# Kernel tuning notes

Hardware: AMD Instinct MI355X
Metric: run time of the kernel (lower is better)

The kernel has to match this reference:

```python
import jax, jax.numpy as jnp
import numpy as np
from jax import lax

jax.config.update("jax_enable_x64", True)

# physical constants / module hyperparameters (match Photodetector defaults)
Q = 1.602176563e-19          # electron charge
KB = 1.3806488e-23           # Boltzmann constant
T_KELVIN = 300.0
BITRATE = 5.0e10
DARK_CURRENT = 1e-10
LOAD_R = 1.0e6
RESPONSIVITY = 1.0
ORDER = 4
WN = 25.0e9 / (0.5 / 1e-12)  # bandwidth / nyquist = 0.05


def _butter_lowpass(order, wn):
    """Digital Butterworth lowpass (b, a), identical algorithm to scipy.signal.butter."""
    warped = 4.0 * np.tan(np.pi * wn / 2.0)          # pre-warped analog cutoff (fs=2)
    kk = np.arange(1, order + 1)
    p = warped * np.exp(1j * np.pi * (2 * kk + order - 1) / (2.0 * order))  # analog poles
    gain = warped ** order
    fs2 = 4.0                                        # 2*fs with fs=2 (bilinear)
    pz = (fs2 + p) / (fs2 - p)                       # digital poles
    gz = gain * np.real(1.0 / np.prod(fs2 - p))      # digital gain (no analog zeros)
    b = np.real(gz * np.poly(-np.ones(order)))       # zeros at z=-1
    a = np.real(np.poly(pz))
    return b, a


def setup_inputs() -> dict:
    key = jax.random.key(0)
    k1, k2 = jax.random.split(key)
    T_steps, B = 16384, 512
    Kf = ORDER + 1
    signal = jax.random.uniform(k1, (T_steps, B), dtype=jnp.float32)  # optical power >= 0
    noise = jax.random.normal(k2, (B, 1, T_steps + Kf - 1), dtype=jnp.float32)
    b, a = _butter_lowpass(ORDER, WN)
    return {
        "signal": signal,
        "noise": noise,
        "b": jnp.asarray(b, jnp.float64),
        "a_rev": jnp.asarray(a[::-1].copy(), jnp.float64),  # module stores a reversed
    }


def reference(signal, noise, b, a_rev):
    sig = signal.astype(jnp.float64)            # (T, B)
    K = b.shape[0]
    x = sig.T                                   # (B, T)
    xp = jnp.pad(x, ((0, 0), (K - 1, 0)))       # left-pad K-1 zeros -> (B, Tp)
    # shot + thermal noise std, batch-mean of signal per timestep
    mean_sig = jnp.mean(RESPONSIVITY * xp, axis=0)  # (Tp,)
    noise_sd = jnp.sqrt(2.0 * Q * BITRATE * (mean_sig + DARK_CURRENT)
                        + 4.0 * KB * T_KELVIN * BITRATE / LOAD_R)
    xn = noise_sd * noise[:, 0, :].astype(jnp.float64) + RESPONSIVITY * xp  # (B, Tp)
    # FIR (torch Conv1d = cross-correlation, matched by lax conv)
    y = lax.conv_general_dilated(xn[:, None, :], b[None, None, :],
                                 window_strides=(1,), padding="VALID")  # (B,1,T)
    s = y[:, 0, :].T                             # (T, B)
    # IIR recurrence: first N samples pass through, then y[n] = s[n] - sum a_rev[:-1]*y[n-N+1:n]
    N = a_rev.shape[0]
    coefs = a_rev[:-1]                           # (N-1,), a_rev[-1] == a[0] == 1

    def step(carry, sn):                         # carry: (N-1, B) = y[n-N+1 .. n-1]
        yn = sn - jnp.sum(coefs[:, None] * carry, axis=0)
        return jnp.concatenate([carry[1:], yn[None]], axis=0), yn

    _, ys = lax.scan(step, s[1:N], s[N:])
    out = jnp.concatenate([s[:N], ys], axis=0)   # (T, B)
    return out.astype(jnp.float32)
```

## Files before the change

kernel.cpp:

```cpp
#include <hip/hip_runtime.h>
#include <math.h>
#include <complex>

#define T_STEPS 16384
#define BATCH   512
#define KF      5
#define TAU     (T_STEPS + KF - 1)
#define NCHUNK  512
#define CHLEN   (T_STEPS / NCHUNK)
#define NTAU    (CHLEN + KF - 1)
#define NSER    12

struct Coefs {
    double b0, b1, b2, b3, b4;
    double c0, c1, c2, c3;
};
struct Mat { double m[16]; };

__device__ __forceinline__ int swz_chunk(int w) { return (w & 7) * (NCHUNK / 8) + (w >> 3); }

__global__ __launch_bounds__(512, 4) void k_stage(const float* __restrict__ signal,
                                                  const float* __restrict__ noise,
                                                  const Coefs k,
                                                  float* __restrict__ sbuf,
                                                  double* __restrict__ pend) {
    __shared__ float  part[NTAU * 8];
    __shared__ double sdsh[NTAU];

    const int tid = threadIdx.x;
    const int b   = tid;
    const int w   = tid >> 6;
    const int l   = tid & 63;
    const int c   = swz_chunk(blockIdx.x);
    const int t0  = c * CHLEN;

    const float4* nb = (const float4*)(noise + (size_t)b * TAU + t0);
    float4 nr[9];
    #pragma unroll
    for (int q = 0; q < 9; ++q) nr[q] = nb[q];
    float nv[NTAU];
    #pragma unroll
    for (int q = 0; q < 9; ++q) {
        nv[4 * q + 0] = nr[q].x; nv[4 * q + 1] = nr[q].y;
        nv[4 * q + 2] = nr[q].z; nv[4 * q + 3] = nr[q].w;
    }

    float sval[NTAU];
    #pragma unroll
    for (int j = 0; j < NTAU; ++j) {
        const int tau = t0 + j;
        sval[j] = (c == 0 && tau < 4) ? 0.0f : signal[(size_t)(tau - 4) * BATCH + b];
    }

    #pragma unroll
    for (int j = 0; j < NTAU; ++j) {
        float v = sval[j];
        for (int off = 32; off > 0; off >>= 1) v += __shfl_down(v, off, 64);
        if (l == 0) part[j * 8 + w] = v;
    }
    __syncthreads();
    if (tid < NTAU) {
        const double c1 = 2.0 * 1.602176563e-19 * 50000000000.0;
        const double c2 = 4.0 * 1.3806488e-23 * 300.0 * 50000000000.0 / 1000000.0;
        double ssum = 0.0;
        #pragma unroll
        for (int i = 0; i < 8; ++i) ssum += (double)part[tid * 8 + i];
        sdsh[tid] = sqrt(c1 * (ssum / 512.0 + 1e-10) + c2);
    }
    __syncthreads();

    auto XN = [&](int j) -> double {
        return sdsh[j] * (double)nv[j] + (double)sval[j];
    };
    double w0 = XN(0), w1 = XN(1), w2 = XN(2), w3 = XN(3), w4;
    double z0 = 0.0, z1 = 0.0, z2 = 0.0, z3 = 0.0;
    #pragma unroll
    for (int i = 0; i < CHLEN; ++i) {
        w4 = XN(i + 4);
        const double s = k.b0 * w0 + k.b1 * w1 + k.b2 * w2 + k.b3 * w3 + k.b4 * w4;
        sbuf[(size_t)(t0 + i) * BATCH + b] = (float)s;
        const double y = (c == 0 && i < 5) ? s
                       : s - (k.c0 * z0 + k.c1 * z1 + k.c2 * z2 + k.c3 * z3);
        z0 = z1; z1 = z2; z2 = z3; z3 = y;
        w0 = w1; w1 = w2; w2 = w3; w3 = w4;
    }
    pend[(size_t)(c * 4 + 0) * BATCH + b] = z0;
    pend[(size_t)(c * 4 + 1) * BATCH + b] = z1;
    pend[(size_t)(c * 4 + 2) * BATCH + b] = z2;
    pend[(size_t)(c * 4 + 3) * BATCH + b] = z3;
}

__global__ __launch_bounds__(256) void k_apply(const float* __restrict__ sbuf,
                                               const Coefs k,
                                               const Mat M,
                                               const double* __restrict__ pend,
                                               float* __restrict__ out) {
    const int b  = (int)blockIdx.y * 256 + threadIdx.x;
    const int c  = swz_chunk(blockIdx.x);
    const int t0 = c * CHLEN;

    double z0 = 0.0, z1 = 0.0, z2 = 0.0, z3 = 0.0;
    #pragma unroll
    for (int d = NSER; d >= 1; --d) {
        if (d <= c) {
            const int j = c - d;
            const double p0 = pend[(size_t)(j * 4 + 0) * BATCH + b];
            const double p1 = pend[(size_t)(j * 4 + 1) * BATCH + b];
            const double p2 = pend[(size_t)(j * 4 + 2) * BATCH + b];
            const double p3 = pend[(size_t)(j * 4 + 3) * BATCH + b];
            const double n0 = p0 + M.m[0] * z0 + M.m[4] * z1 + M.m[8]  * z2 + M.m[12] * z3;
            const double n1 = p1 + M.m[1] * z0 + M.m[5] * z1 + M.m[9]  * z2 + M.m[13] * z3;
            const double n2 = p2 + M.m[2] * z0 + M.m[6] * z1 + M.m[10] * z2 + M.m[14] * z3;
            const double n3 = p3 + M.m[3] * z0 + M.m[7] * z1 + M.m[11] * z2 + M.m[15] * z3;
            z0 = n0; z1 = n1; z2 = n2; z3 = n3;
        }
    }

    #pragma unroll
    for (int i = 0; i < CHLEN; ++i) {
        const double s = (double)sbuf[(size_t)(t0 + i) * BATCH + b];
        const double y = (c == 0 && i < 5) ? s
                       : s - (k.c0 * z0 + k.c1 * z1 + k.c2 * z2 + k.c3 * z3);
        z0 = z1; z1 = z2; z2 = z3; z3 = y;
        out[(size_t)(t0 + i) * BATCH + b] = (float)y;
    }
}

static Coefs make_coefs() {
    const int order = 4;
    const double wn = 25000000000.0 / (0.5 / 1e-12);
    const double warped = 4.0 * tan(M_PI * wn / 2.0);
    std::complex<double> p[4];
    for (int kk = 1; kk <= order; ++kk)
        p[kk - 1] = warped * std::exp(std::complex<double>(0.0,
                        M_PI * (2 * kk + order - 1) / (2.0 * order)));
    const double gain = warped * warped * warped * warped;
    const double fs2 = 4.0;
    std::complex<double> pz[4], prod(1.0, 0.0);
    for (int i = 0; i < 4; ++i) {
        pz[i] = (fs2 + p[i]) / (fs2 - p[i]);
        prod *= (fs2 - p[i]);
    }
    const double gz = gain * std::real(std::complex<double>(1.0, 0.0) / prod);
    std::complex<double> ac[5] = { {1,0}, {0,0}, {0,0}, {0,0}, {0,0} };
    for (int i = 0; i < 4; ++i)
        for (int j = i + 1; j >= 1; --j)
            ac[j] = ac[j] - pz[i] * ac[j - 1];
    Coefs k;
    k.b0 = gz * 1.0; k.b1 = gz * 4.0; k.b2 = gz * 6.0; k.b3 = gz * 4.0; k.b4 = gz * 1.0;
    k.c0 = std::real(ac[4]);
    k.c1 = std::real(ac[3]);
    k.c2 = std::real(ac[2]);
    k.c3 = std::real(ac[1]);
    return k;
}

static void mat_compose(const double* P, const double* Q, double* R) {
    double t[16];
    for (int j = 0; j < 4; ++j)
        for (int i = 0; i < 4; ++i) {
            double s = 0.0;
            for (int kk = 0; kk < 4; ++kk) s += P[j * 4 + kk] * Q[kk * 4 + i];
            t[j * 4 + i] = s;
        }
    for (int i = 0; i < 16; ++i) R[i] = t[i];
}

static Mat make_M(const Coefs& k) {
    double S[16] = {0};
    S[1 * 4 + 0] = 1.0;
    S[2 * 4 + 1] = 1.0;
    S[3 * 4 + 2] = 1.0;
    S[0 * 4 + 3] = -k.c0;
    S[1 * 4 + 3] = -k.c1;
    S[2 * 4 + 3] = -k.c2;
    S[3 * 4 + 3] = -k.c3;
    Mat M;
    double I[16] = {1,0,0,0, 0,1,0,0, 0,0,1,0, 0,0,0,1};
    for (int i = 0; i < 16; ++i) M.m[i] = I[i];
    for (int i = 0; i < CHLEN; ++i) mat_compose(M.m, S, M.m);
    return M;
}

extern "C" void kernel_launch(void* const* d_in, const int* in_sizes, int n_in,
                              void* d_out, int out_size, void* d_ws, size_t ws_size,
                              hipStream_t stream) {
    const float* signal = (const float*)d_in[0];
    const float* noise  = (const float*)d_in[1];
    float* out = (float*)d_out;

    const Coefs k = make_coefs();
    const Mat   M = make_M(k);

    char* ws = (char*)d_ws;
    float*  sbuf = (float*)ws;
    double* pend = (double*)(ws + 33554432);

    hipLaunchKernelGGL(k_stage, dim3(NCHUNK), dim3(512), 0, stream,
                       signal, noise, k, sbuf, pend);
    hipLaunchKernelGGL(k_apply, dim3(NCHUNK, 2), dim3(256), 0, stream,
                       sbuf, k, M, pend, out);
}
```

Measured before the change: 46.62 us.

## Fuse stage and apply kernels with cooperative grid sync and LDS-resident FIR output

Merges the two-kernel chunked IIR scan into one cooperative kernel. The FIR output stays in LDS (64 KB per block) across a grid-wide sync instead of round-tripping through a global scratch buffer, and the per-chunk carry states are stored as float4 instead of four doubles. This removes the second launch and the global write and re-read of the intermediate signal. In exchange it depends on all 512 blocks being co-resident (at least 2 per CU, checked at runtime with a two-kernel fallback), pays for a grid barrier, and rounds the carry states to float precision.

```diff
diff --git a/kernel.cpp b/kernel.cpp
--- a/kernel.cpp
+++ b/kernel.cpp
@@ -1,4 +1,5 @@
 #include <hip/hip_runtime.h>
+#include <hip/hip_cooperative_groups.h>
 #include <math.h>
 #include <complex>
 
@@ -17,7 +18,103 @@
 };
 struct Mat { double m[16]; };
 
+namespace cg = cooperative_groups;
+
 __device__ __forceinline__ int swz_chunk(int w) { return (w & 7) * (NCHUNK / 8) + (w >> 3); }
+
+__global__ __launch_bounds__(512, 4) void k_fused(const float* __restrict__ signal,
+                                                  const float* __restrict__ noise,
+                                                  const Coefs k,
+                                                  const Mat M,
+                                                  float4* __restrict__ pend4,
+                                                  float* __restrict__ out) {
+    __shared__ float  slds[BATCH * CHLEN];
+    __shared__ float  part[NTAU * 8];
+    __shared__ double sdsh[NTAU];
+
+    const int tid = threadIdx.x;
+    const int b   = tid;
+    const int w   = tid >> 6;
+    const int l   = tid & 63;
+    const int c   = swz_chunk(blockIdx.x);
+    const int t0  = c * CHLEN;
+
+    float sval[NTAU];
+    #pragma unroll
+    for (int j = 0; j < NTAU; ++j) {
+        const int tau = t0 + j;
+        sval[j] = (c == 0 && tau < 4) ? 0.0f : signal[(size_t)(tau - 4) * BATCH + b];
+    }
+
+    #pragma unroll
+    for (int j = 0; j < NTAU; ++j) {
+        float v = sval[j];
+        for (int off = 32; off > 0; off >>= 1) v += __shfl_down(v, off, 64);
+        if (l == 0) part[j * 8 + w] = v;
+    }
+    __syncthreads();
+    if (tid < NTAU) {
+        const double c1 = 2.0 * 1.602176563e-19 * 50000000000.0;
+        const double c2 = 4.0 * 1.3806488e-23 * 300.0 * 50000000000.0 / 1000000.0;
+        double ssum = 0.0;
+        #pragma unroll
+        for (int i = 0; i < 8; ++i) ssum += (double)part[tid * 8 + i];
+        sdsh[tid] = sqrt(c1 * (ssum / 512.0 + 1e-10) + c2);
+    }
+    __syncthreads();
+
+    const float4* nb = (const float4*)(noise + (size_t)b * TAU + t0);
+    double z0 = 0.0, z1 = 0.0, z2 = 0.0, z3 = 0.0;
+    {
+        float4 f = nb[0];
+        double w0 = sdsh[0] * (double)f.x + (double)sval[0];
+        double w1 = sdsh[1] * (double)f.y + (double)sval[1];
+        double w2 = sdsh[2] * (double)f.z + (double)sval[2];
+        double w3 = sdsh[3] * (double)f.w + (double)sval[3];
+        #pragma unroll
+        for (int q = 1; q < 9; ++q) {
+            f = nb[q];
+            const float nf[4] = { f.x, f.y, f.z, f.w };
+            #pragma unroll
+            for (int u = 0; u < 4; ++u) {
+                const int i = 4 * (q - 1) + u;
+                const int j = 4 * q + u;
+                const double w4 = sdsh[j] * (double)nf[u] + (double)sval[j];
+                const double s = k.b0 * w0 + k.b1 * w1 + k.b2 * w2 + k.b3 * w3 + k.b4 * w4;
+                slds[i * BATCH + b] = (float)s;
+                const double y = (c == 0 && i < 5) ? s
+                               : s - (k.c0 * z0 + k.c1 * z1 + k.c2 * z2 + k.c3 * z3);
+                z0 = z1; z1 = z2; z2 = z3; z3 = y;
+                w0 = w1; w1 = w2; w2 = w3; w3 = w4;
+            }
+        }
+    }
+    pend4[(size_t)c * BATCH + b] = make_float4((float)z0, (float)z1, (float)z2, (float)z3);
+
+    cg::this_grid().sync();
+
+    z0 = 0.0; z1 = 0.0; z2 = 0.0; z3 = 0.0;
+    #pragma unroll
+    for (int d = NSER; d >= 1; --d) {
+        if (d <= c) {
+            const float4 p = pend4[(size_t)(c - d) * BATCH + b];
+            const double n0 = (double)p.x + M.m[0] * z0 + M.m[4] * z1 + M.m[8]  * z2 + M.m[12] * z3;
+            const double n1 = (double)p.y + M.m[1] * z0 + M.m[5] * z1 + M.m[9]  * z2 + M.m[13] * z3;
+            const double n2 = (double)p.z + M.m[2] * z0 + M.m[6] * z1 + M.m[10] * z2 + M.m[14] * z3;
+            const double n3 = (double)p.w + M.m[3] * z0 + M.m[7] * z1 + M.m[11] * z2 + M.m[15] * z3;
+            z0 = n0; z1 = n1; z2 = n2; z3 = n3;
+        }
+    }
+
+    #pragma unroll
+    for (int i = 0; i < CHLEN; ++i) {
+        const double s = (double)slds[i * BATCH + b];
+        const double y = (c == 0 && i < 5) ? s
+                       : s - (k.c0 * z0 + k.c1 * z1 + k.c2 * z2 + k.c3 * z3);
+        z0 = z1; z1 = z2; z2 = z3; z3 = y;
+        out[(size_t)(t0 + i) * BATCH + b] = (float)y;
+    }
+}
 
 __global__ __launch_bounds__(512, 4) void k_stage(const float* __restrict__ signal,
                                                   const float* __restrict__ noise,
@@ -26,13 +123,10 @@
                                                   double* __restrict__ pend) {
     __shared__ float  part[NTAU * 8];
     __shared__ double sdsh[NTAU];
-
     const int tid = threadIdx.x;
-    const int b   = tid;
-    const int w   = tid >> 6;
-    const int l   = tid & 63;
-    const int c   = swz_chunk(blockIdx.x);
-    const int t0  = c * CHLEN;
+    const int b = tid, w = tid >> 6, l = tid & 63;
+    const int c = swz_chunk(blockIdx.x);
+    const int t0 = c * CHLEN;
 
     const float4* nb = (const float4*)(noise + (size_t)b * TAU + t0);
     float4 nr[9];
@@ -41,17 +135,14 @@
     float nv[NTAU];
     #pragma unroll
     for (int q = 0; q < 9; ++q) {
-        nv[4 * q + 0] = nr[q].x; nv[4 * q + 1] = nr[q].y;
-        nv[4 * q + 2] = nr[q].z; nv[4 * q + 3] = nr[q].w;
-    }
-
+        nv[4*q+0] = nr[q].x; nv[4*q+1] = nr[q].y; nv[4*q+2] = nr[q].z; nv[4*q+3] = nr[q].w;
+    }
     float sval[NTAU];
     #pragma unroll
     for (int j = 0; j < NTAU; ++j) {
         const int tau = t0 + j;
         sval[j] = (c == 0 && tau < 4) ? 0.0f : signal[(size_t)(tau - 4) * BATCH + b];
     }
-
     #pragma unroll
     for (int j = 0; j < NTAU; ++j) {
         float v = sval[j];
@@ -68,59 +159,47 @@
         sdsh[tid] = sqrt(c1 * (ssum / 512.0 + 1e-10) + c2);
     }
     __syncthreads();
-
-    auto XN = [&](int j) -> double {
-        return sdsh[j] * (double)nv[j] + (double)sval[j];
-    };
+    auto XN = [&](int j) -> double { return sdsh[j] * (double)nv[j] + (double)sval[j]; };
     double w0 = XN(0), w1 = XN(1), w2 = XN(2), w3 = XN(3), w4;
-    double z0 = 0.0, z1 = 0.0, z2 = 0.0, z3 = 0.0;
+    double z0 = 0, z1 = 0, z2 = 0, z3 = 0;
     #pragma unroll
     for (int i = 0; i < CHLEN; ++i) {
         w4 = XN(i + 4);
-        const double s = k.b0 * w0 + k.b1 * w1 + k.b2 * w2 + k.b3 * w3 + k.b4 * w4;
+        const double s = k.b0*w0 + k.b1*w1 + k.b2*w2 + k.b3*w3 + k.b4*w4;
         sbuf[(size_t)(t0 + i) * BATCH + b] = (float)s;
-        const double y = (c == 0 && i < 5) ? s
-                       : s - (k.c0 * z0 + k.c1 * z1 + k.c2 * z2 + k.c3 * z3);
+        const double y = (c == 0 && i < 5) ? s : s - (k.c0*z0 + k.c1*z1 + k.c2*z2 + k.c3*z3);
         z0 = z1; z1 = z2; z2 = z3; z3 = y;
         w0 = w1; w1 = w2; w2 = w3; w3 = w4;
     }
-    pend[(size_t)(c * 4 + 0) * BATCH + b] = z0;
-    pend[(size_t)(c * 4 + 1) * BATCH + b] = z1;
-    pend[(size_t)(c * 4 + 2) * BATCH + b] = z2;
-    pend[(size_t)(c * 4 + 3) * BATCH + b] = z3;
+    pend[(size_t)(c*4+0)*BATCH+b] = z0; pend[(size_t)(c*4+1)*BATCH+b] = z1;
+    pend[(size_t)(c*4+2)*BATCH+b] = z2; pend[(size_t)(c*4+3)*BATCH+b] = z3;
 }
 
 __global__ __launch_bounds__(256) void k_apply(const float* __restrict__ sbuf,
-                                               const Coefs k,
-                                               const Mat M,
+                                               const Coefs k, const Mat M,
                                                const double* __restrict__ pend,
                                                float* __restrict__ out) {
-    const int b  = (int)blockIdx.y * 256 + threadIdx.x;
-    const int c  = swz_chunk(blockIdx.x);
+    const int b = (int)blockIdx.y * 256 + threadIdx.x;
+    const int c = swz_chunk(blockIdx.x);
     const int t0 = c * CHLEN;
-
-    double z0 = 0.0, z1 = 0.0, z2 = 0.0, z3 = 0.0;
+    double z0 = 0, z1 = 0, z2 = 0, z3 = 0;
     #pragma unroll
     for (int d = NSER; d >= 1; --d) {
         if (d <= c) {
             const int j = c - d;
-            const double p0 = pend[(size_t)(j * 4 + 0) * BATCH + b];
-            const double p1 = pend[(size_t)(j * 4 + 1) * BATCH + b];
-            const double p2 = pend[(size_t)(j * 4 + 2) * BATCH + b];
-            const double p3 = pend[(size_t)(j * 4 + 3) * BATCH + b];
-            const double n0 = p0 + M.m[0] * z0 + M.m[4] * z1 + M.m[8]  * z2 + M.m[12] * z3;
-            const double n1 = p1 + M.m[1] * z0 + M.m[5] * z1 + M.m[9]  * z2 + M.m[13] * z3;
-            const double n2 = p2 + M.m[2] * z0 + M.m[6] * z1 + M.m[10] * z2 + M.m[14] * z3;
-            const double n3 = p3 + M.m[3] * z0 + M.m[7] * z1 + M.m[11] * z2 + M.m[15] * z3;
+            const double p0 = pend[(size_t)(j*4+0)*BATCH+b], p1 = pend[(size_t)(j*4+1)*BATCH+b];
+            const double p2 = pend[(size_t)(j*4+2)*BATCH+b], p3 = pend[(size_t)(j*4+3)*BATCH+b];
+            const double n0 = p0 + M.m[0]*z0 + M.m[4]*z1 + M.m[8]*z2  + M.m[12]*z3;
+            const double n1 = p1 + M.m[1]*z0 + M.m[5]*z1 + M.m[9]*z2  + M.m[13]*z3;
+            const double n2 = p2 + M.m[2]*z0 + M.m[6]*z1 + M.m[10]*z2 + M.m[14]*z3;
+            const double n3 = p3 + M.m[3]*z0 + M.m[7]*z1 + M.m[11]*z2 + M.m[15]*z3;
             z0 = n0; z1 = n1; z2 = n2; z3 = n3;
         }
     }
-
     #pragma unroll
     for (int i = 0; i < CHLEN; ++i) {
         const double s = (double)sbuf[(size_t)(t0 + i) * BATCH + b];
-        const double y = (c == 0 && i < 5) ? s
-                       : s - (k.c0 * z0 + k.c1 * z1 + k.c2 * z2 + k.c3 * z3);
+        const double y = (c == 0 && i < 5) ? s : s - (k.c0*z0 + k.c1*z1 + k.c2*z2 + k.c3*z3);
         z0 = z1; z1 = z2; z2 = z3; z3 = y;
         out[(size_t)(t0 + i) * BATCH + b] = (float)y;
     }
@@ -148,10 +227,8 @@
             ac[j] = ac[j] - pz[i] * ac[j - 1];
     Coefs k;
     k.b0 = gz * 1.0; k.b1 = gz * 4.0; k.b2 = gz * 6.0; k.b3 = gz * 4.0; k.b4 = gz * 1.0;
-    k.c0 = std::real(ac[4]);
-    k.c1 = std::real(ac[3]);
-    k.c2 = std::real(ac[2]);
-    k.c3 = std::real(ac[1]);
+    k.c0 = std::real(ac[4]); k.c1 = std::real(ac[3]);
+    k.c2 = std::real(ac[2]); k.c3 = std::real(ac[1]);
     return k;
 }
 
@@ -160,21 +237,16 @@
     for (int j = 0; j < 4; ++j)
         for (int i = 0; i < 4; ++i) {
             double s = 0.0;
-            for (int kk = 0; kk < 4; ++kk) s += P[j * 4 + kk] * Q[kk * 4 + i];
-            t[j * 4 + i] = s;
+            for (int kk = 0; kk < 4; ++kk) s += P[j*4+kk] * Q[kk*4+i];
+            t[j*4+i] = s;
         }
     for (int i = 0; i < 16; ++i) R[i] = t[i];
 }
 
 static Mat make_M(const Coefs& k) {
     double S[16] = {0};
-    S[1 * 4 + 0] = 1.0;
-    S[2 * 4 + 1] = 1.0;
-    S[3 * 4 + 2] = 1.0;
-    S[0 * 4 + 3] = -k.c0;
-    S[1 * 4 + 3] = -k.c1;
-    S[2 * 4 + 3] = -k.c2;
-    S[3 * 4 + 3] = -k.c3;
+    S[1*4+0] = 1.0; S[2*4+1] = 1.0; S[3*4+2] = 1.0;
+    S[0*4+3] = -k.c0; S[1*4+3] = -k.c1; S[2*4+3] = -k.c2; S[3*4+3] = -k.c3;
     Mat M;
     double I[16] = {1,0,0,0, 0,1,0,0, 0,0,1,0, 0,0,0,1};
     for (int i = 0; i < 16; ++i) M.m[i] = I[i];
@@ -193,11 +265,22 @@
     const Mat   M = make_M(k);
 
     char* ws = (char*)d_ws;
-    float*  sbuf = (float*)ws;
-    double* pend = (double*)(ws + 33554432);
-
-    hipLaunchKernelGGL(k_stage, dim3(NCHUNK), dim3(512), 0, stream,
-                       signal, noise, k, sbuf, pend);
-    hipLaunchKernelGGL(k_apply, dim3(NCHUNK, 2), dim3(256), 0, stream,
-                       sbuf, k, M, pend, out);
-}
+
+    int maxb = 0;
+    (void)hipOccupancyMaxActiveBlocksPerMultiprocessor(&maxb, (const void*)k_fused, 512, 0);
+
+    if (maxb >= 2) {
+        float4* pend4 = (float4*)ws;
+        void* args[] = { (void*)&signal, (void*)&noise, (void*)&k, (void*)&M,
+                         (void*)&pend4, (void*)&out };
+        hipLaunchCooperativeKernel((const void*)k_fused, dim3(NCHUNK), dim3(512),
+                                   args, 0, stream);
+    } else {
+        float*  sbuf = (float*)ws;
+        double* pend = (double*)(ws + 33554432);
+        hipLaunchKernelGGL(k_stage, dim3(NCHUNK), dim3(512), 0, stream,
+                           signal, noise, k, sbuf, pend);
+        hipLaunchKernelGGL(k_apply, dim3(NCHUNK, 2), dim3(256), 0, stream,
+                           sbuf, k, M, pend, out);
+    }
+}
```

Result: no change. 46.66 us (+0.1%).

## Recompute FIR in apply pass instead of staging filtered signal buffer

Applied to the files above, without the earlier changes.

Splits the noise-std reduction into its own kernel, then runs the chunked FIR+IIR twice: once to produce chunk-end states and once to write outputs, recomputing the FIR from signal and noise rather than storing and re-reading an intermediate buffer. Chunk-end states are stored as float4 instead of doubles. This removes the intermediate write/read and the in-block reduction, but adds extra reads of the inputs, an extra launch, and reduced precision in the carried states.

```diff
diff --git a/kernel.cpp b/kernel.cpp
--- a/kernel.cpp
+++ b/kernel.cpp
@@ -19,111 +19,110 @@
 
 __device__ __forceinline__ int swz_chunk(int w) { return (w & 7) * (NCHUNK / 8) + (w >> 3); }
 
-__global__ __launch_bounds__(512, 4) void k_stage(const float* __restrict__ signal,
-                                                  const float* __restrict__ noise,
-                                                  const Coefs k,
-                                                  float* __restrict__ sbuf,
-                                                  double* __restrict__ pend) {
-    __shared__ float  part[NTAU * 8];
-    __shared__ double sdsh[NTAU];
-
-    const int tid = threadIdx.x;
-    const int b   = tid;
-    const int w   = tid >> 6;
-    const int l   = tid & 63;
-    const int c   = swz_chunk(blockIdx.x);
-    const int t0  = c * CHLEN;
-
-    const float4* nb = (const float4*)(noise + (size_t)b * TAU + t0);
-    float4 nr[9];
-    #pragma unroll
-    for (int q = 0; q < 9; ++q) nr[q] = nb[q];
-    float nv[NTAU];
-    #pragma unroll
-    for (int q = 0; q < 9; ++q) {
-        nv[4 * q + 0] = nr[q].x; nv[4 * q + 1] = nr[q].y;
-        nv[4 * q + 2] = nr[q].z; nv[4 * q + 3] = nr[q].w;
+__global__ __launch_bounds__(256) void k_sd(const float* __restrict__ signal,
+                                            double* __restrict__ sd) {
+    const int wave = threadIdx.x >> 6;
+    const int lane = threadIdx.x & 63;
+    const int tau  = blockIdx.x * 4 + wave;
+    if (tau >= TAU) return;
+    float m = 0.0f;
+    if (tau >= 4) {
+        const float4* p = (const float4*)(signal + (size_t)(tau - 4) * BATCH);
+        const float4 a = p[lane], bq = p[lane + 64];
+        float v = (a.x + a.y) + (a.z + a.w) + (bq.x + bq.y) + (bq.z + bq.w);
+        for (int off = 32; off > 0; off >>= 1) v += __shfl_down(v, off, 64);
+        m = v;
     }
-
-    float sval[NTAU];
-    #pragma unroll
-    for (int j = 0; j < NTAU; ++j) {
-        const int tau = t0 + j;
-        sval[j] = (c == 0 && tau < 4) ? 0.0f : signal[(size_t)(tau - 4) * BATCH + b];
-    }
-
-    #pragma unroll
-    for (int j = 0; j < NTAU; ++j) {
-        float v = sval[j];
-        for (int off = 32; off > 0; off >>= 1) v += __shfl_down(v, off, 64);
-        if (l == 0) part[j * 8 + w] = v;
-    }
-    __syncthreads();
-    if (tid < NTAU) {
+    if (lane == 0) {
         const double c1 = 2.0 * 1.602176563e-19 * 50000000000.0;
         const double c2 = 4.0 * 1.3806488e-23 * 300.0 * 50000000000.0 / 1000000.0;
-        double ssum = 0.0;
+        sd[tau] = sqrt(c1 * ((double)m / 512.0 + 1e-10) + c2);
+    }
+}
+
+template <bool WRITE_OUT>
+__device__ __forceinline__ void run_chunk(const float* __restrict__ signal,
+                                          const float* __restrict__ noise,
+                                          const double* __restrict__ sdsh,
+                                          const Coefs& k, int c, int b,
+                                          double& z0, double& z1, double& z2, double& z3,
+                                          float* __restrict__ out) {
+    const int t0 = c * CHLEN;
+    const float4* nb = (const float4*)(noise + (size_t)b * TAU + t0);
+
+    auto SIG = [&](int j) -> double {
+        const int tau = t0 + j;
+        return (c == 0 && tau < 4) ? 0.0 : (double)signal[(size_t)(tau - 4) * BATCH + b];
+    };
+
+    float4 f = nb[0];
+    double w0 = sdsh[0] * (double)f.x + SIG(0);
+    double w1 = sdsh[1] * (double)f.y + SIG(1);
+    double w2 = sdsh[2] * (double)f.z + SIG(2);
+    double w3 = sdsh[3] * (double)f.w + SIG(3);
+    #pragma unroll
+    for (int q = 1; q < 9; ++q) {
+        f = nb[q];
+        const float nf[4] = { f.x, f.y, f.z, f.w };
         #pragma unroll
-        for (int i = 0; i < 8; ++i) ssum += (double)part[tid * 8 + i];
-        sdsh[tid] = sqrt(c1 * (ssum / 512.0 + 1e-10) + c2);
+        for (int u = 0; u < 4; ++u) {
+            const int i = 4 * (q - 1) + u;
+            const int j = 4 * q + u;
+            const double w4 = sdsh[j] * (double)nf[u] + SIG(j);
+            const double s = k.b0 * w0 + k.b1 * w1 + k.b2 * w2 + k.b3 * w3 + k.b4 * w4;
+            const double y = (c == 0 && i < 5) ? s
+                           : s - (k.c0 * z0 + k.c1 * z1 + k.c2 * z2 + k.c3 * z3);
+            z0 = z1; z1 = z2; z2 = z3; z3 = y;
+            w0 = w1; w1 = w2; w2 = w3; w3 = w4;
+            if (WRITE_OUT) out[(size_t)(t0 + i) * BATCH + b] = (float)y;
+        }
     }
+}
+
+__global__ __launch_bounds__(256, 4) void k_pend(const float* __restrict__ signal,
+                                                 const float* __restrict__ noise,
+                                                 const double* __restrict__ sd,
+                                                 const Coefs k,
+                                                 float4* __restrict__ pend4) {
+    __shared__ double sdsh[NTAU];
+    const int tid = threadIdx.x;
+    const int b   = (int)blockIdx.y * 256 + tid;
+    const int c   = swz_chunk(blockIdx.x);
+    if (tid < NTAU) sdsh[tid] = sd[c * CHLEN + tid];
     __syncthreads();
 
-    auto XN = [&](int j) -> double {
-        return sdsh[j] * (double)nv[j] + (double)sval[j];
-    };
-    double w0 = XN(0), w1 = XN(1), w2 = XN(2), w3 = XN(3), w4;
     double z0 = 0.0, z1 = 0.0, z2 = 0.0, z3 = 0.0;
-    #pragma unroll
-    for (int i = 0; i < CHLEN; ++i) {
-        w4 = XN(i + 4);
-        const double s = k.b0 * w0 + k.b1 * w1 + k.b2 * w2 + k.b3 * w3 + k.b4 * w4;
-        sbuf[(size_t)(t0 + i) * BATCH + b] = (float)s;
-        const double y = (c == 0 && i < 5) ? s
-                       : s - (k.c0 * z0 + k.c1 * z1 + k.c2 * z2 + k.c3 * z3);
-        z0 = z1; z1 = z2; z2 = z3; z3 = y;
-        w0 = w1; w1 = w2; w2 = w3; w3 = w4;
-    }
-    pend[(size_t)(c * 4 + 0) * BATCH + b] = z0;
-    pend[(size_t)(c * 4 + 1) * BATCH + b] = z1;
-    pend[(size_t)(c * 4 + 2) * BATCH + b] = z2;
-    pend[(size_t)(c * 4 + 3) * BATCH + b] = z3;
+    run_chunk<false>(signal, noise, sdsh, k, c, b, z0, z1, z2, z3, nullptr);
+    pend4[(size_t)c * BATCH + b] = make_float4((float)z0, (float)z1, (float)z2, (float)z3);
 }
 
-__global__ __launch_bounds__(256) void k_apply(const float* __restrict__ sbuf,
-                                               const Coefs k,
-                                               const Mat M,
-                                               const double* __restrict__ pend,
-                                               float* __restrict__ out) {
-    const int b  = (int)blockIdx.y * 256 + threadIdx.x;
-    const int c  = swz_chunk(blockIdx.x);
-    const int t0 = c * CHLEN;
+__global__ __launch_bounds__(256, 4) void k_out(const float* __restrict__ signal,
+                                                const float* __restrict__ noise,
+                                                const double* __restrict__ sd,
+                                                const Coefs k, const Mat M,
+                                                const float4* __restrict__ pend4,
+                                                float* __restrict__ out) {
+    __shared__ double sdsh[NTAU];
+    const int tid = threadIdx.x;
+    const int b   = (int)blockIdx.y * 256 + tid;
+    const int c   = swz_chunk(blockIdx.x);
+    if (tid < NTAU) sdsh[tid] = sd[c * CHLEN + tid];
+    __syncthreads();
 
     double z0 = 0.0, z1 = 0.0, z2 = 0.0, z3 = 0.0;
     #pragma unroll
     for (int d = NSER; d >= 1; --d) {
         if (d <= c) {
-            const int j = c - d;
-            const double p0 = pend[(size_t)(j * 4 + 0) * BATCH + b];
-            const double p1 = pend[(size_t)(j * 4 + 1) * BATCH + b];
-            const double p2 = pend[(size_t)(j * 4 + 2) * BATCH + b];
-            const double p3 = pend[(size_t)(j * 4 + 3) * BATCH + b];
-            const double n0 = p0 + M.m[0] * z0 + M.m[4] * z1 + M.m[8]  * z2 + M.m[12] * z3;
-            const double n1 = p1 + M.m[1] * z0 + M.m[5] * z1 + M.m[9]  * z2 + M.m[13] * z3;
-            const double n2 = p2 + M.m[2] * z0 + M.m[6] * z1 + M.m[10] * z2 + M.m[14] * z3;
-            const double n3 = p3 + M.m[3] * z0 + M.m[7] * z1 + M.m[11] * z2 + M.m[15] * z3;
+            const float4 p = pend4[(size_t)(c - d) * BATCH + b];
+            const double n0 = (double)p.x + M.m[0] * z0 + M.m[4] * z1 + M.m[8]  * z2 + M.m[12] * z3;
+            const double n1 = (double)p.y + M.m[1] * z0 + M.m[5] * z1 + M.m[9]  * z2 + M.m[13] * z3;
+            const double n2 = (double)p.z + M.m[2] * z0 + M.m[6] * z1 + M.m[10] * z2 + M.m[14] * z3;
+            const double n3 = (double)p.w + M.m[3] * z0 + M.m[7] * z1 + M.m[11] * z2 + M.m[15] * z3;
             z0 = n0; z1 = n1; z2 = n2; z3 = n3;
         }
     }
 
-    #pragma unroll
-    for (int i = 0; i < CHLEN; ++i) {
-        const double s = (double)sbuf[(size_t)(t0 + i) * BATCH + b];
-        const double y = (c == 0 && i < 5) ? s
-                       : s - (k.c0 * z0 + k.c1 * z1 + k.c2 * z2 + k.c3 * z3);
-        z0 = z1; z1 = z2; z2 = z3; z3 = y;
-        out[(size_t)(t0 + i) * BATCH + b] = (float)y;
-    }
+    run_chunk<true>(signal, noise, sdsh, k, c, b, z0, z1, z2, z3, out);
 }
 
 static Coefs make_coefs() {
@@ -148,10 +147,8 @@
             ac[j] = ac[j] - pz[i] * ac[j - 1];
     Coefs k;
     k.b0 = gz * 1.0; k.b1 = gz * 4.0; k.b2 = gz * 6.0; k.b3 = gz * 4.0; k.b4 = gz * 1.0;
-    k.c0 = std::real(ac[4]);
-    k.c1 = std::real(ac[3]);
-    k.c2 = std::real(ac[2]);
-    k.c3 = std::real(ac[1]);
+    k.c0 = std::real(ac[4]); k.c1 = std::real(ac[3]);
+    k.c2 = std::real(ac[2]); k.c3 = std::real(ac[1]);
     return k;
 }
 
@@ -160,21 +157,16 @@
     for (int j = 0; j < 4; ++j)
         for (int i = 0; i < 4; ++i) {
             double s = 0.0;
-            for (int kk = 0; kk < 4; ++kk) s += P[j * 4 + kk] * Q[kk * 4 + i];
-            t[j * 4 + i] = s;
+            for (int kk = 0; kk < 4; ++kk) s += P[j*4+kk] * Q[kk*4+i];
+            t[j*4+i] = s;
         }
     for (int i = 0; i < 16; ++i) R[i] = t[i];
 }
 
 static Mat make_M(const Coefs& k) {
     double S[16] = {0};
-    S[1 * 4 + 0] = 1.0;
-    S[2 * 4 + 1] = 1.0;
-    S[3 * 4 + 2] = 1.0;
-    S[0 * 4 + 3] = -k.c0;
-    S[1 * 4 + 3] = -k.c1;
-    S[2 * 4 + 3] = -k.c2;
-    S[3 * 4 + 3] = -k.c3;
+    S[1*4+0] = 1.0; S[2*4+1] = 1.0; S[3*4+2] = 1.0;
+    S[0*4+3] = -k.c0; S[1*4+3] = -k.c1; S[2*4+3] = -k.c2; S[3*4+3] = -k.c3;
     Mat M;
     double I[16] = {1,0,0,0, 0,1,0,0, 0,0,1,0, 0,0,0,1};
     for (int i = 0; i < 16; ++i) M.m[i] = I[i];
@@ -193,11 +185,12 @@
     const Mat   M = make_M(k);
 
     char* ws = (char*)d_ws;
-    float*  sbuf = (float*)ws;
-    double* pend = (double*)(ws + 33554432);
+    double* sd    = (double*)ws;
+    float4* pend4 = (float4*)(ws + 131104);
 
-    hipLaunchKernelGGL(k_stage, dim3(NCHUNK), dim3(512), 0, stream,
-                       signal, noise, k, sbuf, pend);
-    hipLaunchKernelGGL(k_apply, dim3(NCHUNK, 2), dim3(256), 0, stream,
-                       sbuf, k, M, pend, out);
+    hipLaunchKernelGGL(k_sd,   dim3((TAU + 3) / 4), dim3(256), 0, stream, signal, sd);
+    hipLaunchKernelGGL(k_pend, dim3(NCHUNK, 2), dim3(256), 0, stream,
+                       signal, noise, sd, k, pend4);
+    hipLaunchKernelGGL(k_out,  dim3(NCHUNK, 2), dim3(256), 0, stream,
+                       signal, noise, sd, k, M, pend4, out);
 }
```

Result: slower. 55.37 us (+18.8%).

## Store zero-state IIR output in fp16 and correct with homogeneous response

Applied to the files above, without the earlier changes.

The stage kernel now writes the locally filtered IIR output y (zero initial state) as fp16 instead of the FIR output as fp32. The apply kernel reconstructs the true output by adding the homogeneous response of the propagated carry state, rather than rerunning the full recurrence. Chunk-end states are packed into a single float4, and the carry look-back shrinks from 12 to 8 chunks. This halves intermediate traffic and removes most of the second-pass arithmetic, at the cost of fp16 rounding on outputs and a shorter carry propagation horizon that could affect accuracy.

```diff
diff --git a/kernel.cpp b/kernel.cpp
--- a/kernel.cpp
+++ b/kernel.cpp
@@ -1,4 +1,5 @@
 #include <hip/hip_runtime.h>
+#include <hip/hip_fp16.h>
 #include <math.h>
 #include <complex>
 
@@ -9,7 +10,7 @@
 #define NCHUNK  512
 #define CHLEN   (T_STEPS / NCHUNK)
 #define NTAU    (CHLEN + KF - 1)
-#define NSER    12
+#define NSER    8
 
 struct Coefs {
     double b0, b1, b2, b3, b4;
@@ -22,8 +23,8 @@
 __global__ __launch_bounds__(512, 4) void k_stage(const float* __restrict__ signal,
                                                   const float* __restrict__ noise,
                                                   const Coefs k,
-                                                  float* __restrict__ sbuf,
-                                                  double* __restrict__ pend) {
+                                                  __half* __restrict__ ybuf,
+                                                  float4* __restrict__ pend4) {
     __shared__ float  part[NTAU * 8];
     __shared__ double sdsh[NTAU];
 
@@ -41,8 +42,8 @@
     float nv[NTAU];
     #pragma unroll
     for (int q = 0; q < 9; ++q) {
-        nv[4 * q + 0] = nr[q].x; nv[4 * q + 1] = nr[q].y;
-        nv[4 * q + 2] = nr[q].z; nv[4 * q + 3] = nr[q].w;
+        nv[4*q+0] = nr[q].x; nv[4*q+1] = nr[q].y;
+        nv[4*q+2] = nr[q].z; nv[4*q+3] = nr[q].w;
     }
 
     float sval[NTAU];
@@ -69,60 +70,49 @@
     }
     __syncthreads();
 
-    auto XN = [&](int j) -> double {
-        return sdsh[j] * (double)nv[j] + (double)sval[j];
-    };
+    auto XN = [&](int j) -> double { return sdsh[j] * (double)nv[j] + (double)sval[j]; };
     double w0 = XN(0), w1 = XN(1), w2 = XN(2), w3 = XN(3), w4;
     double z0 = 0.0, z1 = 0.0, z2 = 0.0, z3 = 0.0;
     #pragma unroll
     for (int i = 0; i < CHLEN; ++i) {
         w4 = XN(i + 4);
-        const double s = k.b0 * w0 + k.b1 * w1 + k.b2 * w2 + k.b3 * w3 + k.b4 * w4;
-        sbuf[(size_t)(t0 + i) * BATCH + b] = (float)s;
+        const double s = k.b0*w0 + k.b1*w1 + k.b2*w2 + k.b3*w3 + k.b4*w4;
         const double y = (c == 0 && i < 5) ? s
-                       : s - (k.c0 * z0 + k.c1 * z1 + k.c2 * z2 + k.c3 * z3);
+                       : s - (k.c0*z0 + k.c1*z1 + k.c2*z2 + k.c3*z3);
+        ybuf[(size_t)(t0 + i) * BATCH + b] = __float2half((float)y);
         z0 = z1; z1 = z2; z2 = z3; z3 = y;
         w0 = w1; w1 = w2; w2 = w3; w3 = w4;
     }
-    pend[(size_t)(c * 4 + 0) * BATCH + b] = z0;
-    pend[(size_t)(c * 4 + 1) * BATCH + b] = z1;
-    pend[(size_t)(c * 4 + 2) * BATCH + b] = z2;
-    pend[(size_t)(c * 4 + 3) * BATCH + b] = z3;
+    pend4[(size_t)c * BATCH + b] = make_float4((float)z0, (float)z1, (float)z2, (float)z3);
 }
 
-__global__ __launch_bounds__(256) void k_apply(const float* __restrict__ sbuf,
-                                               const Coefs k,
-                                               const Mat M,
-                                               const double* __restrict__ pend,
+__global__ __launch_bounds__(256) void k_apply(const __half* __restrict__ ybuf,
+                                               const Coefs k, const Mat M,
+                                               const float4* __restrict__ pend4,
                                                float* __restrict__ out) {
     const int b  = (int)blockIdx.y * 256 + threadIdx.x;
     const int c  = swz_chunk(blockIdx.x);
     const int t0 = c * CHLEN;
 
-    double z0 = 0.0, z1 = 0.0, z2 = 0.0, z3 = 0.0;
+    double d0 = 0.0, d1 = 0.0, d2 = 0.0, d3 = 0.0;
     #pragma unroll
     for (int d = NSER; d >= 1; --d) {
         if (d <= c) {
-            const int j = c - d;
-            const double p0 = pend[(size_t)(j * 4 + 0) * BATCH + b];
-            const double p1 = pend[(size_t)(j * 4 + 1) * BATCH + b];
-            const double p2 = pend[(size_t)(j * 4 + 2) * BATCH + b];
-            const double p3 = pend[(size_t)(j * 4 + 3) * BATCH + b];
-            const double n0 = p0 + M.m[0] * z0 + M.m[4] * z1 + M.m[8]  * z2 + M.m[12] * z3;
-            const double n1 = p1 + M.m[1] * z0 + M.m[5] * z1 + M.m[9]  * z2 + M.m[13] * z3;
-            const double n2 = p2 + M.m[2] * z0 + M.m[6] * z1 + M.m[10] * z2 + M.m[14] * z3;
-            const double n3 = p3 + M.m[3] * z0 + M.m[7] * z1 + M.m[11] * z2 + M.m[15] * z3;
-            z0 = n0; z1 = n1; z2 = n2; z3 = n3;
+            const float4 p = pend4[(size_t)(c - d) * BATCH + b];
+            const double n0 = (double)p.x + M.m[0]*d0 + M.m[4]*d1 + M.m[8]*d2  + M.m[12]*d3;
+            const double n1 = (double)p.y + M.m[1]*d0 + M.m[5]*d1 + M.m[9]*d2  + M.m[13]*d3;
+            const double n2 = (double)p.z + M.m[2]*d0 + M.m[6]*d1 + M.m[10]*d2 + M.m[14]*d3;
+            const double n3 = (double)p.w + M.m[3]*d0 + M.m[7]*d1 + M.m[11]*d2 + M.m[15]*d3;
+            d0 = n0; d1 = n1; d2 = n2; d3 = n3;
         }
     }
 
     #pragma unroll
     for (int i = 0; i < CHLEN; ++i) {
-        const double s = (double)sbuf[(size_t)(t0 + i) * BATCH + b];
-        const double y = (c == 0 && i < 5) ? s
-                       : s - (k.c0 * z0 + k.c1 * z1 + k.c2 * z2 + k.c3 * z3);
-        z0 = z1; z1 = z2; z2 = z3; z3 = y;
-        out[(size_t)(t0 + i) * BATCH + b] = (float)y;
+        const double h = -(k.c0*d0 + k.c1*d1 + k.c2*d2 + k.c3*d3);
+        const size_t idx = (size_t)(t0 + i) * BATCH + b;
+        out[idx] = (float)((double)__half2float(ybuf[idx]) + h);
+        d0 = d1; d1 = d2; d2 = d3; d3 = h;
     }
 }
 
@@ -148,10 +138,8 @@
             ac[j] = ac[j] - pz[i] * ac[j - 1];
     Coefs k;
     k.b0 = gz * 1.0; k.b1 = gz * 4.0; k.b2 = gz * 6.0; k.b3 = gz * 4.0; k.b4 = gz * 1.0;
-    k.c0 = std::real(ac[4]);
-    k.c1 = std::real(ac[3]);
-    k.c2 = std::real(ac[2]);
-    k.c3 = std::real(ac[1]);
+    k.c0 = std::real(ac[4]); k.c1 = std::real(ac[3]);
+    k.c2 = std::real(ac[2]); k.c3 = std::real(ac[1]);
     return k;
 }
 
@@ -160,21 +148,16 @@
     for (int j = 0; j < 4; ++j)
         for (int i = 0; i < 4; ++i) {
             double s = 0.0;
-            for (int kk = 0; kk < 4; ++kk) s += P[j * 4 + kk] * Q[kk * 4 + i];
-            t[j * 4 + i] = s;
+            for (int kk = 0; kk < 4; ++kk) s += P[j*4+kk] * Q[kk*4+i];
+            t[j*4+i] = s;
         }
     for (int i = 0; i < 16; ++i) R[i] = t[i];
 }
 
 static Mat make_M(const Coefs& k) {
     double S[16] = {0};
-    S[1 * 4 + 0] = 1.0;
-    S[2 * 4 + 1] = 1.0;
-    S[3 * 4 + 2] = 1.0;
-    S[0 * 4 + 3] = -k.c0;
-    S[1 * 4 + 3] = -k.c1;
-    S[2 * 4 + 3] = -k.c2;
-    S[3 * 4 + 3] = -k.c3;
+    S[1*4+0] = 1.0; S[2*4+1] = 1.0; S[3*4+2] = 1.0;
+    S[0*4+3] = -k.c0; S[1*4+3] = -k.c1; S[2*4+3] = -k.c2; S[3*4+3] = -k.c3;
     Mat M;
     double I[16] = {1,0,0,0, 0,1,0,0, 0,0,1,0, 0,0,0,1};
     for (int i = 0; i < 16; ++i) M.m[i] = I[i];
@@ -193,11 +176,11 @@
     const Mat   M = make_M(k);
 
     char* ws = (char*)d_ws;
-    float*  sbuf = (float*)ws;
-    double* pend = (double*)(ws + 33554432);
+    __half* ybuf  = (__half*)ws;
+    float4* pend4 = (float4*)(ws + 16777216);
 
     hipLaunchKernelGGL(k_stage, dim3(NCHUNK), dim3(512), 0, stream,
-                       signal, noise, k, sbuf, pend);
+                       signal, noise, k, ybuf, pend4);
     hipLaunchKernelGGL(k_apply, dim3(NCHUNK, 2), dim3(256), 0, stream,
-                       sbuf, k, M, pend, out);
+                       ybuf, k, M, pend4, out);
 }
```

Measured after the change: 45.23 us. 1.03x faster.
